# Performance work log

Hardware: AMD Instinct MI355X
Metric: run time of the kernel (lower is better)

## Reference

```python
import jax, jax.numpy as jnp
import numpy as np

B, W, G, E, NI, K = 2048, 8192, 8, 128, 16, 15


def setup_inputs() -> dict:
    key = jax.random.key(0)
    ks = jax.random.split(key, 12)
    wavelengths_nm = jnp.linspace(300.0, 400.0, W, dtype=jnp.float32)
    # Rayleigh optical depth (Hansen & Travis style approximation), AMF=1 column
    lam_um = wavelengths_nm / 1000.0
    rayleigh_od = (0.008569 * lam_um ** -4
                   * (1.0 + 0.0113 * lam_um ** -2 + 0.00013 * lam_um ** -4)).astype(jnp.float32)
    return {
        "gas_columns": jax.random.uniform(ks[0], (B, G), jnp.float32),
        "instrument_ids": jax.random.randint(ks[1], (B,), 0, NI),
        "nuisance_latent": jax.random.normal(ks[2], (B, G), jnp.float32),
        "air_mass": 1.0 + 2.0 * jax.random.uniform(ks[3], (B,), jnp.float32),
        "wavelengths_nm": wavelengths_nm,
        "absorption": 0.1 * jax.random.uniform(ks[4], (G, W), jnp.float32),
        "continuum_basis": 0.05 * jax.random.normal(ks[5], (G + 1, W), jnp.float32),
        "rayleigh_od": rayleigh_od,
        "embed_table": jax.random.normal(ks[6], (NI, E), jnp.float32),
        "w1": jax.random.normal(ks[7], (E + G, 64), jnp.float32) / np.sqrt(E + G),
        "b1": jnp.zeros((64,), jnp.float32),
        "w2": jax.random.normal(ks[8], (64, 7), jnp.float32) / 8.0,
        "b2": jnp.zeros((7,), jnp.float32),
    }


def _gaussian_kernel(width_px, kernel_size):
    half = (kernel_size - 1) / 2
    pos = jnp.linspace(-half, half, kernel_size, dtype=width_px.dtype)  # [K]
    k = jnp.exp(-0.5 * (pos[None, :] / (width_px[:, None] + 1e-6)) ** 2)  # [B,K]
    return k / k.sum(axis=1, keepdims=True)


def _forward(gas_columns, nuisance_latent, air_mass, wavelengths_nm, absorption,
             continuum_basis, rayleigh_od, embed_table, w1, b1, w2, b2,
             instrument_ids):
    b = gas_columns.shape[0]
    am = air_mass[:, None]                                   # [B,1]
    scaled = gas_columns * am                                # [B,G]
    optical_depth = scaled @ absorption                      # [B,W]
    ones = jnp.ones((b, 1), gas_columns.dtype)
    continuum = jnp.concatenate([gas_columns, ones], axis=1) @ continuum_basis  # [B,W]
    differential = optical_depth + continuum + am * rayleigh_od[None, :]

    # nuisance MLP on [latent, embedding]
    embed = embed_table[instrument_ids]                      # [B,E]
    nin = jnp.concatenate([nuisance_latent, embed], axis=-1)
    h = jax.nn.gelu(nin @ w1 + b1, approximate=False)
    p = h @ w2 + b2                                          # [B,7]

    gain = jax.nn.softplus(p[:, 0]) + 0.001
    offset = p[:, 1]
    woff = 0.05 * jnp.tanh(p[:, 2])
    wscale = 1.0 + 0.005 * jnp.tanh(p[:, 3])
    lsf = jnp.clip(jax.nn.softplus(p[:, 4]) + 0.001, 0.2, 5.0)
    stray = jax.nn.sigmoid(p[:, 5]) * 0.05
    nonlin = 0.02 * jnp.tanh(p[:, 6])

    # per-sample wavelength shift/scale + linear resampling
    new_wl = wavelengths_nm[None, :] * wscale[:, None] + woff[:, None]  # [B,W]
    differential = jax.vmap(lambda wq, d: jnp.interp(wq, wavelengths_nm, d))(new_wl, differential)

    # per-sample Gaussian LSF convolution (replicate padding)
    kernel = _gaussian_kernel(lsf, K)                        # [B,K]
    pad = K // 2
    padded = jnp.pad(differential, ((0, 0), (pad, pad)), mode='edge')  # [B,W+K-1]
    n = differential.shape[1]
    convolved = sum(padded[:, k:k + n] * kernel[:, k:k + 1] for k in range(K))

    counts = jnp.exp(-convolved)
    post = gain[:, None] * counts + offset[:, None]
    total_nl = jnp.clip(nonlin, -0.04, 0.04)                 # instrument nonlinearity = 0
    nl_counts = post + total_nl[:, None] * post ** 2
    total_stray = jnp.clip(stray, 0.0, 0.2)                  # instrument stray = 0
    simulated = (1.0 - total_stray[:, None]) * nl_counts \
        + total_stray[:, None] * nl_counts.mean(axis=1, keepdims=True)
    return simulated


def reference(gas_columns, instrument_ids, nuisance_latent, air_mass,
              wavelengths_nm, absorption, continuum_basis, rayleigh_od,
              embed_table, w1, b1, w2, b2):
    return _forward(gas_columns, nuisance_latent, air_mass, wavelengths_nm,
                    absorption, continuum_basis, rayleigh_od, embed_table,
                    w1, b1, w2, b2, instrument_ids)
```

## Files before the change

### kernel.cpp

```cpp
#include <hip/hip_runtime.h>

#define W_ 8192
#define NBATCH 2048
#define NT 512
#define WPB 8
#define SEG 1024
#define IRW 544
#define NCHW 2

typedef unsigned short u16_t;
typedef _Float16 h2v __attribute__((ext_vector_type(2)));

__device__ __forceinline__ u16_t f2h(float x){ _Float16 h=(_Float16)x; return __builtin_bit_cast(u16_t,h); }
__device__ __forceinline__ float h2f(u16_t u){ return (float)__builtin_bit_cast(_Float16,u); }
__device__ __forceinline__ unsigned pk2(float a,float b){ return (unsigned)f2h(a)|((unsigned)f2h(b)<<16); }
__device__ __forceinline__ float dot2u(unsigned a,unsigned b,float c){
#if __has_builtin(__builtin_amdgcn_fdot2)
  return __builtin_amdgcn_fdot2(__builtin_bit_cast(h2v,a),__builtin_bit_cast(h2v,b),c,false);
#else
  h2v ha=__builtin_bit_cast(h2v,a), hb=__builtin_bit_cast(h2v,b);
  return c+(float)ha[0]*(float)hb[0]+(float)ha[1]*(float)hb[1];
#endif
}
__device__ __forceinline__ unsigned pkrtz(float a,float b){
#if __has_builtin(__builtin_amdgcn_cvt_pkrtz)
  return __builtin_bit_cast(unsigned, __builtin_amdgcn_cvt_pkrtz(a,b));
#else
  return pk2(a,b);
#endif
}
__device__ __forceinline__ unsigned alignb(unsigned hi, unsigned lo){
#if __has_builtin(__builtin_amdgcn_alignbit)
  return __builtin_amdgcn_alignbit(hi, lo, 16);
#else
  return (lo >> 16) | (hi << 16);
#endif
}
__device__ __forceinline__ float softplusf(float x){ return fmaxf(x,0.f)+log1pf(expf(-fabsf(x))); }
__device__ __forceinline__ unsigned rflv(unsigned v){
  return (unsigned)__builtin_amdgcn_readfirstlane((int)v);
}

__global__ __launch_bounds__(256, 2)
void doas_prep(const float* __restrict__ absn, const float* __restrict__ cbn,
               const float* __restrict__ ray, const int* __restrict__ iid,
               const float* __restrict__ nuis, const float* __restrict__ emb,
               const float* __restrict__ w1, const float* __restrict__ b1,
               const float* __restrict__ w2, const float* __restrict__ b2,
               unsigned* __restrict__ Tp, float* __restrict__ params){
  const int tid = threadIdx.x;
  const int b = blockIdx.x;
  __shared__ float hS[4][64];
  __shared__ float pS[4][8];

  if (b < 32){
    const int w = b*256 + tid;
    #pragma unroll
    for (int q=0;q<4;++q) Tp[q*W_+w]     = pk2(absn[(2*q)*W_+w], absn[(2*q+1)*W_+w]);
    #pragma unroll
    for (int q=0;q<4;++q) Tp[(4+q)*W_+w] = pk2(cbn[(2*q)*W_+w],  cbn[(2*q+1)*W_+w]);
    Tp[8*W_+w] = pk2(cbn[8*W_+w], ray[w]);
  }

  {
    const int rl = tid >> 6, j = tid & 63;
    const int r = b*4 + rl;
    const int id = iid[r];
    float acc = b1[j];
    const float* nrow = nuis + (size_t)r * 8;
    #pragma unroll
    for (int i = 0; i < 8; ++i) acc = fmaf(nrow[i], w1[i*64 + j], acc);
    const float* erow = emb + (size_t)id * 128;
    for (int i = 0; i < 128; ++i) acc = fmaf(erow[i], w1[(8+i)*64 + j], acc);
    hS[rl][j] = 0.5f * acc * (1.0f + erff(acc * 0.70710678118654752f));
  }
  __syncthreads();
  if (tid < 4*7){
    const int rl = tid / 7, k = tid % 7;
    float p = b2[k];
    for (int j = 0; j < 64; ++j) p = fmaf(hS[rl][j], w2[j*7+k], p);
    pS[rl][k] = p;
  }
  __syncthreads();
  if (tid < 4){
    const int rl = tid;
    const int r = b*4 + rl;
    float p0=pS[rl][0], p1=pS[rl][1], p2=pS[rl][2], p3=pS[rl][3],
          p4=pS[rl][4], p5=pS[rl][5], p6=pS[rl][6];
    float gainv = softplusf(p0) + 0.001f;
    float offv  = p1;
    float woffv = 0.05f * tanhf(p2);
    float wscv  = 1.0f + 0.005f * tanhf(p3);
    float lsf   = fminf(fmaxf(softplusf(p4) + 0.001f, 0.2f), 5.0f);
    float strv  = fminf(fmaxf((1.0f/(1.0f+expf(-p5))) * 0.05f, 0.0f), 0.2f);
    float nlin  = fminf(fmaxf(0.02f * tanhf(p6), -0.04f), 0.04f);
    float iw = 1.0f/(lsf + 1e-6f);
    float ks[15]; float ksum = 0.f;
    #pragma unroll
    for (int k2=0;k2<15;++k2){ float pp=(float)(k2-7)*iw; float e=expf(-0.5f*pp*pp); ks[k2]=e; ksum+=e; }
    float inv = 1.0f/ksum;
    float* pr = params + (size_t)r*16;
    unsigned* pu = (unsigned*)pr;
    #pragma unroll
    for (int i=0;i<7;++i) pu[i] = pk2(ks[2*i]*inv, ks[2*i+1]*inv);
    pu[7] = pk2(ks[14]*inv, 0.0f);
    pu[8] = pk2(0.0f, ks[14]*inv);
    pr[9]  = wscv;
    pr[10] = (300.0f*(wscv - 1.0f) + woffv) * (8191.0f/100.0f);
    pr[11] = gainv; pr[12] = offv; pr[13] = nlin; pr[14] = strv;
    pr[15] = 0.f;
  }
}

__global__ __launch_bounds__(256, 2)
void doas_diff(const unsigned* __restrict__ Tp, const float* __restrict__ gas,
               const float* __restrict__ air, u16_t* __restrict__ diffG){
  const int tid = threadIdx.x;
  const int e0 = blockIdx.x*512 + 2*tid;
  const int r0 = blockIdx.y*4;
  unsigned csgA[4][9];
  #pragma unroll
  for (int rr=0;rr<4;++rr){
    const float am = air[r0+rr];
    const float* gfp = gas + (size_t)(r0+rr)*8;
    #pragma unroll
    for (int q=0;q<4;++q) csgA[rr][q]   = rflv(pk2(gfp[2*q]*am, gfp[2*q+1]*am));
    #pragma unroll
    for (int q=0;q<4;++q) csgA[rr][4+q] = rflv(pk2(gfp[2*q],    gfp[2*q+1]));
    csgA[rr][8] = rflv(pk2(1.0f, am));
  }
  uint2 dq[9];
  #pragma unroll
  for (int q=0;q<9;++q) dq[q] = *(const uint2*)(Tp + q*W_ + e0);
  #pragma unroll
  for (int rr=0;rr<4;++rr){
    float a0=0.f, a1=0.f;
    #pragma unroll
    for (int q=0;q<9;++q){
      a0 = dot2u(dq[q].x, csgA[rr][q], a0);
      a1 = dot2u(dq[q].y, csgA[rr][q], a1);
    }
    ((unsigned*)diffG)[((size_t)(r0+rr)*W_ + e0)>>1] = pkrtz(a0, a1);
  }
}

template<bool CLO, bool CHI>
__device__ __forceinline__ void interp_chunk(int cbase, int l, const unsigned* __restrict__ rU,
                                             unsigned* __restrict__ irowU,
                                             float wscale, float posoff){
  #pragma unroll
  for (int it=0; it<5; ++it){
    const int pi = it*64 + l;
    if (pi < 264){
      float v2[2];
      #pragma unroll
      for (int u=0;u<2;++u){
        int j = cbase + 2*pi + u;
        if (CLO) j = max(j, 0);
        if (CHI) j = min(j, W_-1);
        float pos = fmaf((float)j, wscale, posoff);
        if (CLO) pos = fmaxf(pos, 0.0f);
        if (CHI) pos = fminf(pos, 8191.0f);
        int i0 = (int)pos;
        if (CHI) i0 = min(i0, W_-2);
        const float fr = pos - (float)i0;
        const int m = i0 >> 1;
        const unsigned u0 = rU[m];
        const unsigned u1 = rU[m+1];
        const unsigned hu0 = u0 >> 16;
        const bool odd = (i0 & 1);
        const unsigned ua = odd ? hu0 : u0;
        const unsigned ub = odd ? u1  : hu0;
        const float d0 = h2f((u16_t)ua);
        const float d1 = h2f((u16_t)ub);
        v2[u] = fmaf(fr, d1-d0, d0);
      }
      irowU[pi] = pkrtz(v2[0], v2[1]);
    }
  }
}

__global__ __launch_bounds__(NT, 2)
void doas_main2(const float* __restrict__ params, const u16_t* __restrict__ diffG,
                float* __restrict__ out){
  __shared__ u16_t rowH[W_ + 16];
  __shared__ u16_t irowS[WPB][IRW];
  __shared__ float wsumS[WPB];

  const int tid = threadIdx.x;
  const int row = blockIdx.x;

  {
    const uint4* dg4 = (const uint4*)(diffG + (size_t)row * W_);
    uint4* r4 = (uint4*)rowH;
    r4[tid]      = dg4[tid];
    r4[tid+512]  = dg4[tid+512];
  }

  const float* pr = params + (size_t)row * 16;
  const unsigned* pu = (const unsigned*)pr;
  unsigned kwp[7];
  #pragma unroll
  for (int i=0;i<7;++i) kwp[i] = pu[i];
  const unsigned k14lo = pu[7], k14hi = pu[8];
  const float wscale = pr[9],  posoff = pr[10];
  const float gainv  = pr[11], offv   = pr[12];
  const float nlin   = pr[13], strv   = pr[14];

  __syncthreads();

  const int wid = tid >> 6, l = tid & 63;
  const int segbase = wid * SEG;
  const unsigned* rU = (const unsigned*)rowH;
  u16_t* irow = &irowS[wid][0];
  unsigned* irowU = (unsigned*)irow;

  float accsum = 0.f;
  unsigned nlp[NCHW][4];

  #pragma unroll
  for (int c = 0; c < NCHW; ++c) {
    const int cbase = segbase + (c << 9) - 8;
    if (wid == 0 && c == 0)
      interp_chunk<true,false>(cbase, l, rU, irowU, wscale, posoff);
    else if (wid == WPB-1 && c == NCHW-1)
      interp_chunk<false,true>(cbase, l, rU, irowU, wscale, posoff);
    else
      interp_chunk<false,false>(cbase, l, rU, irowU, wscale, posoff);
    __builtin_amdgcn_wave_barrier();
    {
      const uint4* qp = (const uint4*)irow + l;
      const uint4 A = qp[0], B = qp[1], C = qp[2];
      unsigned q[12] = {A.x,A.y,A.z,A.w, B.x,B.y,B.z,B.w, C.x,C.y,C.z,C.w};
      unsigned sh[10];
      #pragma unroll
      for (int m=0;m<10;++m) sh[m] = alignb(q[m+1], q[m]);
      float nlv[8];
      #pragma unroll
      for (int t=0;t<8;++t){
        const int s2 = t >> 1;
        float cv = 0.f;
        if ((t & 1) == 0){
          #pragma unroll
          for (int i=0;i<7;++i) cv = dot2u(sh[s2+i], kwp[i], cv);
          cv = dot2u(q[s2+7], k14hi, cv);
        } else {
          #pragma unroll
          for (int i=0;i<7;++i) cv = dot2u(q[s2+1+i], kwp[i], cv);
          cv = dot2u(q[s2+8], k14lo, cv);
        }
        const float counts = __expf(-cv);
        const float post = fmaf(gainv, counts, offv);
        const float v = fmaf(nlin*post, post, post);
        accsum += v;
        nlv[t] = v;
      }
      nlp[c][0] = pkrtz(nlv[0], nlv[1]);
      nlp[c][1] = pkrtz(nlv[2], nlv[3]);
      nlp[c][2] = pkrtz(nlv[4], nlv[5]);
      nlp[c][3] = pkrtz(nlv[6], nlv[7]);
    }
    __builtin_amdgcn_wave_barrier();
  }

  float s = accsum;
  #pragma unroll
  for (int off2 = 32; off2 >= 1; off2 >>= 1) s += __shfl_down(s, off2);
  if (l == 0) wsumS[wid] = s;
  __syncthreads();
  const float meanv = (wsumS[0]+wsumS[1]+wsumS[2]+wsumS[3]
                      +wsumS[4]+wsumS[5]+wsumS[6]+wsumS[7]) * (1.0f/8192.0f);

  {
    const float aa = 1.0f - strv;
    const float bb = strv * meanv;
    float* orow = out + (size_t)row * W_;
    #pragma unroll
    for (int c = 0; c < NCHW; ++c) {
      const unsigned u0 = nlp[c][0], u1 = nlp[c][1], u2 = nlp[c][2], u3 = nlp[c][3];
      float4 o0, o1;
      o0.x = fmaf(aa, h2f((u16_t)(u0 & 0xffffu)), bb);
      o0.y = fmaf(aa, h2f((u16_t)(u0 >> 16)),     bb);
      o0.z = fmaf(aa, h2f((u16_t)(u1 & 0xffffu)), bb);
      o0.w = fmaf(aa, h2f((u16_t)(u1 >> 16)),     bb);
      o1.x = fmaf(aa, h2f((u16_t)(u2 & 0xffffu)), bb);
      o1.y = fmaf(aa, h2f((u16_t)(u2 >> 16)),     bb);
      o1.z = fmaf(aa, h2f((u16_t)(u3 & 0xffffu)), bb);
      o1.w = fmaf(aa, h2f((u16_t)(u3 >> 16)),     bb);
      float* dst = orow + segbase + (c << 9) + 8*l;
      *(float4*)(dst)     = o0;
      *(float4*)(dst + 4) = o1;
    }
  }
}

__global__ __launch_bounds__(256, 2)
void doas_mono(const float* __restrict__ gas, const int* __restrict__ iid,
               const float* __restrict__ nuis, const float* __restrict__ air,
               const float* __restrict__ absn, const float* __restrict__ cbn,
               const float* __restrict__ ray, const float* __restrict__ emb,
               const float* __restrict__ w1, const float* __restrict__ b1,
               const float* __restrict__ w2, const float* __restrict__ b2,
               float* __restrict__ out)
{
  __shared__ u16_t ringS[4][2048];
  __shared__ u16_t irowS[4][IRW];
  __shared__ float hS[64];
  __shared__ float pS[8];
  __shared__ float scalS[52];
  __shared__ float wsumS[4];

  const int tid = threadIdx.x;
  const int row = blockIdx.x;

  if (tid < 64) {
    const int j = tid;
    const int id = iid[row];
    float acc = b1[j];
    const float* nrow = nuis + (size_t)row * 8;
    #pragma unroll
    for (int i = 0; i < 8; ++i) acc = fmaf(nrow[i], w1[i*64 + j], acc);
    const float* erow = emb + (size_t)id * 128;
    for (int i = 0; i < 128; ++i) acc = fmaf(erow[i], w1[(8+i)*64 + j], acc);
    hS[j] = 0.5f * acc * (1.0f + erff(acc * 0.70710678118654752f));
  }
  __syncthreads();
  if (tid < 7) {
    float p = b2[tid];
    for (int j = 0; j < 64; ++j) p = fmaf(hS[j], w2[j*7+tid], p);
    pS[tid] = p;
  }
  __syncthreads();
  if (tid == 0) {
    float p0=pS[0], p1=pS[1], p2=pS[2], p3=pS[3], p4=pS[4], p5=pS[5], p6=pS[6];
    float gainv = softplusf(p0) + 0.001f;
    float offv  = p1;
    float woffv = 0.05f * tanhf(p2);
    float wscv  = 1.0f + 0.005f * tanhf(p3);
    float lsf   = fminf(fmaxf(softplusf(p4) + 0.001f, 0.2f), 5.0f);
    float strv  = fminf(fmaxf((1.0f/(1.0f+expf(-p5))) * 0.05f, 0.0f), 0.2f);
    float nlin  = fminf(fmaxf(0.02f * tanhf(p6), -0.04f), 0.04f);
    float iw = 1.0f/(lsf + 1e-6f);
    float ks[15]; float ksum = 0.f;
    #pragma unroll
    for (int k2=0;k2<15;++k2){ float pp=(float)(k2-7)*iw; float e=expf(-0.5f*pp*pp); ks[k2]=e; ksum+=e; }
    float inv = 1.0f/ksum;
    scalS[15] = wscv;
    scalS[16] = (300.0f*(wscv - 1.0f) + woffv) * (8191.0f/100.0f);
    scalS[17] = gainv; scalS[18] = offv; scalS[19] = nlin; scalS[20] = strv;
    scalS[22] = air[row];
    unsigned* su = (unsigned*)scalS;
    #pragma unroll
    for (int i=0;i<7;++i) su[32+i] = pk2(ks[2*i]*inv, ks[2*i+1]*inv);
    su[39] = pk2(ks[14]*inv, 0.0f);
    su[40] = pk2(0.0f, ks[14]*inv);
    #pragma unroll
    for (int g=0; g<8; ++g) scalS[23+g] = gas[(size_t)row*8+g];
  }
  __syncthreads();

  const int wid = tid >> 6, l = tid & 63;
  const int segbase = wid * 2048;
  const unsigned* scalU = (const unsigned*)scalS;
  unsigned kwp[7];
  #pragma unroll
  for (int i=0;i<7;++i) kwp[i] = rflv(scalU[32+i]);
  const unsigned k14lo = rflv(scalU[39]), k14hi = rflv(scalU[40]);
  const float wscale = scalS[15], posoff = scalS[16];
  const float gainv  = scalS[17], offv   = scalS[18];
  const float nlin   = scalS[19], strv   = scalS[20];

  u16_t* ring = &ringS[wid][0];
  unsigned* ringU = (unsigned*)ring;
  u16_t* irow = &irowS[wid][0];
  unsigned* irowU = (unsigned*)irow;

  auto do_diff = [&](int s){
    const int sbase = segbase - 256 + (s << 9);
    #pragma unroll
    for (int it=0; it<4; ++it){
      const int e0 = sbase + ((it*64 + l) << 1);
      const int eL = min(max(e0, 0), W_-2);
      const float am = scalS[22];
      float a0=0.f, a1=0.f;
      #pragma unroll
      for (int g=0; g<8; ++g){
        const float cg = scalS[23+g];
        const float ca = cg*am;
        a0 = fmaf(ca, absn[g*W_+eL],   a0); a0 = fmaf(cg, cbn[g*W_+eL],   a0);
        a1 = fmaf(ca, absn[g*W_+eL+1], a1); a1 = fmaf(cg, cbn[g*W_+eL+1], a1);
      }
      a0 += cbn[8*W_+eL]   + am*ray[eL];
      a1 += cbn[8*W_+eL+1] + am*ray[eL+1];
      ringU[((unsigned)e0 & 2047) >> 1] = pkrtz(a0, a1);
    }
  };

  float accsum = 0.f;
  unsigned nlp[4][4];

  do_diff(0); do_diff(1);
  __builtin_amdgcn_wave_barrier();

  #pragma unroll
  for (int c = 0; c < 4; ++c) {
    if (c < 3) do_diff(c+2);
    __builtin_amdgcn_wave_barrier();
    {
      const int cbase = segbase + (c << 9) - 8;
      #pragma unroll
      for (int it = 0; it < 5; ++it) {
        const int pi = it*64 + l;
        if (pi < 264) {
          float v2[2];
          #pragma unroll
          for (int u=0; u<2; ++u){
            const int j = cbase + 2*pi + u;
            const int jc = min(max(j, 0), W_-1);
            float pos = fmaf((float)jc, wscale, posoff);
            pos = fminf(fmaxf(pos, 0.0f), 8191.0f);
            const int i0 = min((int)pos, W_-2);
            const float fr = pos - (float)i0;
            const float d0 = h2f(ring[ i0    & 2047]);
            const float d1 = h2f(ring[(i0+1) & 2047]);
            v2[u] = fmaf(fr, d1-d0, d0);
          }
          irowU[pi] = pkrtz(v2[0], v2[1]);
        }
      }
    }
    __builtin_amdgcn_wave_barrier();
    {
      const uint4* qp = (const uint4*)irow + l;
      const uint4 A = qp[0], B = qp[1], C = qp[2];
      unsigned q[12] = {A.x,A.y,A.z,A.w, B.x,B.y,B.z,B.w, C.x,C.y,C.z,C.w};
      unsigned sh[10];
      #pragma unroll
      for (int m=0;m<10;++m) sh[m] = alignb(q[m+1], q[m]);
      float nlv[8];
      #pragma unroll
      for (int t=0;t<8;++t){
        const int s2 = t >> 1;
        float cv = 0.f;
        if ((t & 1) == 0){
          #pragma unroll
          for (int i=0;i<7;++i) cv = dot2u(sh[s2+i], kwp[i], cv);
          cv = dot2u(q[s2+7], k14hi, cv);
        } else {
          #pragma unroll
          for (int i=0;i<7;++i) cv = dot2u(q[s2+1+i], kwp[i], cv);
          cv = dot2u(q[s2+8], k14lo, cv);
        }
        const float counts = __expf(-cv);
        const float post = fmaf(gainv, counts, offv);
        const float v = fmaf(nlin*post, post, post);
        accsum += v;
        nlv[t] = v;
      }
      nlp[c][0] = pkrtz(nlv[0], nlv[1]);
      nlp[c][1] = pkrtz(nlv[2], nlv[3]);
      nlp[c][2] = pkrtz(nlv[4], nlv[5]);
      nlp[c][3] = pkrtz(nlv[6], nlv[7]);
    }
    __builtin_amdgcn_wave_barrier();
  }

  float s = accsum;
  #pragma unroll
  for (int off2 = 32; off2 >= 1; off2 >>= 1) s += __shfl_down(s, off2);
  if (l == 0) wsumS[wid] = s;
  __syncthreads();
  const float meanv = (wsumS[0]+wsumS[1]+wsumS[2]+wsumS[3]) * (1.0f/8192.0f);

  {
    const float aa = 1.0f - strv;
    const float bb = strv * meanv;
    float* orow = out + (size_t)row * W_;
    #pragma unroll
    for (int c = 0; c < 4; ++c) {
      const unsigned u0 = nlp[c][0], u1 = nlp[c][1], u2 = nlp[c][2], u3 = nlp[c][3];
      float4 o0, o1;
      o0.x = fmaf(aa, h2f((u16_t)(u0 & 0xffffu)), bb);
      o0.y = fmaf(aa, h2f((u16_t)(u0 >> 16)),     bb);
      o0.z = fmaf(aa, h2f((u16_t)(u1 & 0xffffu)), bb);
      o0.w = fmaf(aa, h2f((u16_t)(u1 >> 16)),     bb);
      o1.x = fmaf(aa, h2f((u16_t)(u2 & 0xffffu)), bb);
      o1.y = fmaf(aa, h2f((u16_t)(u2 >> 16)),     bb);
      o1.z = fmaf(aa, h2f((u16_t)(u3 & 0xffffu)), bb);
      o1.w = fmaf(aa, h2f((u16_t)(u3 >> 16)),     bb);
      float* dst = orow + segbase + (c << 9) + 8*l;
      *(float4*)(dst)     = o0;
      *(float4*)(dst + 4) = o1;
    }
  }
}

extern "C" void kernel_launch(void* const* d_in, const int* in_sizes, int n_in,
                              void* d_out, int out_size, void* d_ws, size_t ws_size,
                              hipStream_t stream) {
  const float* gas  = (const float*)d_in[0];
  const int*   iid  = (const int*)d_in[1];
  const float* nuis = (const float*)d_in[2];
  const float* air  = (const float*)d_in[3];
  const float* wl   = (const float*)d_in[4];
  const float* absn = (const float*)d_in[5];
  const float* cbn  = (const float*)d_in[6];
  const float* ray  = (const float*)d_in[7];
  const float* emb  = (const float*)d_in[8];
  const float* w1   = (const float*)d_in[9];
  const float* b1   = (const float*)d_in[10];
  const float* w2   = (const float*)d_in[11];
  const float* b2   = (const float*)d_in[12];
  float* out = (float*)d_out;
  (void)in_sizes; (void)n_in; (void)out_size; (void)wl;

  const size_t packBytes = (size_t)9 * W_ * 4;
  const size_t parBytes  = (size_t)NBATCH * 16 * 4;
  const size_t diffBytes = (size_t)NBATCH * W_ * 2;

  if (ws_size >= packBytes + parBytes + diffBytes) {
    unsigned* Tp  = (unsigned*)d_ws;
    float* params = (float*)((char*)d_ws + packBytes);
    u16_t* diffG  = (u16_t*)((char*)d_ws + packBytes + parBytes);
    hipLaunchKernelGGL(doas_prep, dim3(NBATCH/4), dim3(256), 0, stream,
                       absn, cbn, ray, iid, nuis, emb, w1, b1, w2, b2, Tp, params);
    hipLaunchKernelGGL(doas_diff, dim3(W_/512, NBATCH/4), dim3(256), 0, stream,
                       Tp, gas, air, diffG);
    hipLaunchKernelGGL(doas_main2, dim3(NBATCH), dim3(NT), 0, stream,
                       params, diffG, out);
  } else {
    hipLaunchKernelGGL(doas_mono, dim3(NBATCH), dim3(256), 0, stream,
                       gas, iid, nuis, air, absn, cbn, ray, emb, w1, b1, w2, b2, out);
  }
}
```

Baseline: 64.28 us.

## Fuse differential spectrum computation into main kernel, two rows per block

Removes the separate doas_diff kernel and its fp16 global scratch buffer: the main kernel now computes each row's differential optical depth directly into shared memory from the packed absorption table. Each block handles two rows (4 waves per row, 4 chunks each), which amortises the table loads across rows. Per-row parameters are made wave-uniform with readfirstlane. This removes a launch and a full round trip of a 32 MB intermediate through global memory. In exchange the block uses more shared memory (32 KB row buffer) and does the dot-product work inline, which may lower occupancy.

```diff
diff --git a/kernel.cpp b/kernel.cpp
--- a/kernel.cpp
+++ b/kernel.cpp
@@ -3,10 +3,9 @@
 #define W_ 8192
 #define NBATCH 2048
 #define NT 512
-#define WPB 8
-#define SEG 1024
+#define RPB 2
 #define IRW 544
-#define NCHW 2
+#define NCHW 4
 
 typedef unsigned short u16_t;
 typedef _Float16 h2v __attribute__((ext_vector_type(2)));
@@ -39,6 +38,9 @@
 __device__ __forceinline__ float softplusf(float x){ return fmaxf(x,0.f)+log1pf(expf(-fabsf(x))); }
 __device__ __forceinline__ unsigned rflv(unsigned v){
   return (unsigned)__builtin_amdgcn_readfirstlane((int)v);
+}
+__device__ __forceinline__ float rflvf(float v){
+  return __builtin_bit_cast(float, __builtin_amdgcn_readfirstlane(__builtin_bit_cast(int, v)));
 }
 
 __global__ __launch_bounds__(256, 2)
@@ -109,38 +111,6 @@
     pr[10] = (300.0f*(wscv - 1.0f) + woffv) * (8191.0f/100.0f);
     pr[11] = gainv; pr[12] = offv; pr[13] = nlin; pr[14] = strv;
     pr[15] = 0.f;
-  }
-}
-
-__global__ __launch_bounds__(256, 2)
-void doas_diff(const unsigned* __restrict__ Tp, const float* __restrict__ gas,
-               const float* __restrict__ air, u16_t* __restrict__ diffG){
-  const int tid = threadIdx.x;
-  const int e0 = blockIdx.x*512 + 2*tid;
-  const int r0 = blockIdx.y*4;
-  unsigned csgA[4][9];
-  #pragma unroll
-  for (int rr=0;rr<4;++rr){
-    const float am = air[r0+rr];
-    const float* gfp = gas + (size_t)(r0+rr)*8;
-    #pragma unroll
-    for (int q=0;q<4;++q) csgA[rr][q]   = rflv(pk2(gfp[2*q]*am, gfp[2*q+1]*am));
-    #pragma unroll
-    for (int q=0;q<4;++q) csgA[rr][4+q] = rflv(pk2(gfp[2*q],    gfp[2*q+1]));
-    csgA[rr][8] = rflv(pk2(1.0f, am));
-  }
-  uint2 dq[9];
-  #pragma unroll
-  for (int q=0;q<9;++q) dq[q] = *(const uint2*)(Tp + q*W_ + e0);
-  #pragma unroll
-  for (int rr=0;rr<4;++rr){
-    float a0=0.f, a1=0.f;
-    #pragma unroll
-    for (int q=0;q<9;++q){
-      a0 = dot2u(dq[q].x, csgA[rr][q], a0);
-      a1 = dot2u(dq[q].y, csgA[rr][q], a1);
-    }
-    ((unsigned*)diffG)[((size_t)(r0+rr)*W_ + e0)>>1] = pkrtz(a0, a1);
   }
 }
 
@@ -181,39 +151,74 @@
 }
 
 __global__ __launch_bounds__(NT, 2)
-void doas_main2(const float* __restrict__ params, const u16_t* __restrict__ diffG,
+void doas_main3(const unsigned* __restrict__ Tp, const float* __restrict__ gas,
+                const float* __restrict__ air, const float* __restrict__ params,
                 float* __restrict__ out){
-  __shared__ u16_t rowH[W_ + 16];
-  __shared__ u16_t irowS[WPB][IRW];
-  __shared__ float wsumS[WPB];
+  __shared__ u16_t rowH[RPB*W_ + 16];
+  __shared__ u16_t irowS[8][IRW];
+  __shared__ float wsumS[8];
 
   const int tid = threadIdx.x;
-  const int row = blockIdx.x;
-
-  {
-    const uint4* dg4 = (const uint4*)(diffG + (size_t)row * W_);
-    uint4* r4 = (uint4*)rowH;
-    r4[tid]      = dg4[tid];
-    r4[tid+512]  = dg4[tid+512];
-  }
-
-  const float* pr = params + (size_t)row * 16;
+  const int r0 = blockIdx.x * RPB;
+
+  unsigned csg[RPB][9];
+  #pragma unroll
+  for (int rr=0; rr<RPB; ++rr){
+    const float am = air[r0+rr];
+    const float* gfp = gas + (size_t)(r0+rr)*8;
+    #pragma unroll
+    for (int q=0;q<4;++q) csg[rr][q]   = rflv(pk2(gfp[2*q]*am, gfp[2*q+1]*am));
+    #pragma unroll
+    for (int q=0;q<4;++q) csg[rr][4+q] = rflv(pk2(gfp[2*q],    gfp[2*q+1]));
+    csg[rr][8] = rflv(pk2(1.0f, am));
+  }
+
+  unsigned* rowHU = (unsigned*)rowH;
+  #pragma unroll
+  for (int it=0; it<4; ++it){
+    const int e0 = it*2048 + tid*4;
+    uint4 dq[9];
+    #pragma unroll
+    for (int q=0;q<9;++q) dq[q] = *(const uint4*)(Tp + q*W_ + e0);
+    float a[RPB][4];
+    #pragma unroll
+    for (int rr=0;rr<RPB;++rr){ a[rr][0]=0.f; a[rr][1]=0.f; a[rr][2]=0.f; a[rr][3]=0.f; }
+    #pragma unroll
+    for (int q=0;q<9;++q){
+      #pragma unroll
+      for (int rr=0;rr<RPB;++rr){
+        a[rr][0] = dot2u(dq[q].x, csg[rr][q], a[rr][0]);
+        a[rr][1] = dot2u(dq[q].y, csg[rr][q], a[rr][1]);
+        a[rr][2] = dot2u(dq[q].z, csg[rr][q], a[rr][2]);
+        a[rr][3] = dot2u(dq[q].w, csg[rr][q], a[rr][3]);
+      }
+    }
+    #pragma unroll
+    for (int rr=0;rr<RPB;++rr){
+      uint2 wv = make_uint2(pkrtz(a[rr][0],a[rr][1]), pkrtz(a[rr][2],a[rr][3]));
+      *(uint2*)(rowHU + ((rr*W_ + e0) >> 1)) = wv;
+    }
+  }
+
+  const int wid = tid >> 6, l = tid & 63;
+  const int row  = wid >> 2;
+  const int sidx = wid & 3;
+  const float* pr = params + (size_t)(r0 + row) * 16;
   const unsigned* pu = (const unsigned*)pr;
   unsigned kwp[7];
   #pragma unroll
-  for (int i=0;i<7;++i) kwp[i] = pu[i];
-  const unsigned k14lo = pu[7], k14hi = pu[8];
-  const float wscale = pr[9],  posoff = pr[10];
-  const float gainv  = pr[11], offv   = pr[12];
-  const float nlin   = pr[13], strv   = pr[14];
-
-  __syncthreads();
-
-  const int wid = tid >> 6, l = tid & 63;
-  const int segbase = wid * SEG;
-  const unsigned* rU = (const unsigned*)rowH;
+  for (int i=0;i<7;++i) kwp[i] = rflv(pu[i]);
+  const unsigned k14lo = rflv(pu[7]), k14hi = rflv(pu[8]);
+  const float wscale = rflvf(pr[9]),  posoff = rflvf(pr[10]);
+  const float gainv  = rflvf(pr[11]), offv   = rflvf(pr[12]);
+  const float nlin   = rflvf(pr[13]), strv   = rflvf(pr[14]);
+
+  __syncthreads();
+
+  const unsigned* rU = (const unsigned*)(rowH + row*W_);
   u16_t* irow = &irowS[wid][0];
   unsigned* irowU = (unsigned*)irow;
+  const int segbase = sidx * 2048;
 
   float accsum = 0.f;
   unsigned nlp[NCHW][4];
@@ -221,9 +226,9 @@
   #pragma unroll
   for (int c = 0; c < NCHW; ++c) {
     const int cbase = segbase + (c << 9) - 8;
-    if (wid == 0 && c == 0)
+    if (sidx == 0 && c == 0)
       interp_chunk<true,false>(cbase, l, rU, irowU, wscale, posoff);
-    else if (wid == WPB-1 && c == NCHW-1)
+    else if (sidx == 3 && c == NCHW-1)
       interp_chunk<false,true>(cbase, l, rU, irowU, wscale, posoff);
     else
       interp_chunk<false,false>(cbase, l, rU, irowU, wscale, posoff);
@@ -268,13 +273,13 @@
   for (int off2 = 32; off2 >= 1; off2 >>= 1) s += __shfl_down(s, off2);
   if (l == 0) wsumS[wid] = s;
   __syncthreads();
-  const float meanv = (wsumS[0]+wsumS[1]+wsumS[2]+wsumS[3]
-                      +wsumS[4]+wsumS[5]+wsumS[6]+wsumS[7]) * (1.0f/8192.0f);
+  const float meanv = (wsumS[row*4+0]+wsumS[row*4+1]+wsumS[row*4+2]+wsumS[row*4+3])
+                      * (1.0f/8192.0f);
 
   {
     const float aa = 1.0f - strv;
     const float bb = strv * meanv;
-    float* orow = out + (size_t)row * W_;
+    float* orow = out + (size_t)(r0 + row) * W_;
     #pragma unroll
     for (int c = 0; c < NCHW; ++c) {
       const unsigned u0 = nlp[c][0], u1 = nlp[c][1], u2 = nlp[c][2], u3 = nlp[c][3];
@@ -516,18 +521,14 @@
 
   const size_t packBytes = (size_t)9 * W_ * 4;
   const size_t parBytes  = (size_t)NBATCH * 16 * 4;
-  const size_t diffBytes = (size_t)NBATCH * W_ * 2;
-
-  if (ws_size >= packBytes + parBytes + diffBytes) {
+
+  if (ws_size >= packBytes + parBytes) {
     unsigned* Tp  = (unsigned*)d_ws;
     float* params = (float*)((char*)d_ws + packBytes);
-    u16_t* diffG  = (u16_t*)((char*)d_ws + packBytes + parBytes);
     hipLaunchKernelGGL(doas_prep, dim3(NBATCH/4), dim3(256), 0, stream,
                        absn, cbn, ray, iid, nuis, emb, w1, b1, w2, b2, Tp, params);
-    hipLaunchKernelGGL(doas_diff, dim3(W_/512, NBATCH/4), dim3(256), 0, stream,
-                       Tp, gas, air, diffG);
-    hipLaunchKernelGGL(doas_main2, dim3(NBATCH), dim3(NT), 0, stream,
-                       params, diffG, out);
+    hipLaunchKernelGGL(doas_main3, dim3(NBATCH/RPB), dim3(NT), 0, stream,
+                       Tp, gas, air, params, out);
   } else {
     hipLaunchKernelGGL(doas_mono, dim3(NBATCH), dim3(256), 0, stream,
                        gas, iid, nuis, air, absn, cbn, ray, emb, w1, b1, w2, b2, out);
```

New measurement: 55.33 us. -13.9%, faster.
